# Kernel optimization log

Hardware: AMD Instinct MI355X
Metric: run time of the kernel (lower is better)

## Reference

```python
import jax, jax.numpy as jnp
import numpy as np

N_NODES = 50000
N_EDGES = 800000
D = 128
BN_EPS = 1e-5


def swish(h):
    return h * jax.nn.sigmoid(h)


def linear_bn_swish(h, W, b, g, be):
    # Linear -> BatchNorm1d (training stats, biased var) -> Swish
    h = h @ W + b
    mean = jnp.mean(h, axis=0)
    var = jnp.mean((h - mean) ** 2, axis=0)
    h = (h - mean) * jax.lax.rsqrt(var + BN_EPS) * g + be
    return swish(h)


def setup_inputs() -> dict:
    key = jax.random.key(0)
    ks = jax.random.split(key, 8)
    scale = 1.0 / np.sqrt(D)
    return {
        "x": jax.random.normal(ks[0], (N_NODES, D), dtype=jnp.float32),
        "vals": jax.random.uniform(ks[1], (N_EDGES,), dtype=jnp.float32),
        "W1": jax.random.normal(ks[2], (D, D), dtype=jnp.float32) * scale,
        "b1": jnp.zeros((D,), dtype=jnp.float32),
        "g1": jnp.ones((D,), dtype=jnp.float32),
        "be1": jnp.zeros((D,), dtype=jnp.float32),
        "W2": jax.random.normal(ks[3], (D, D), dtype=jnp.float32) * scale,
        "b2": jnp.zeros((D,), dtype=jnp.float32),
        "g2": jnp.ones((D,), dtype=jnp.float32),
        "be2": jnp.zeros((D,), dtype=jnp.float32),
        "eps": jnp.zeros((1,), dtype=jnp.float32),
        "rows": jax.random.randint(ks[4], (N_EDGES,), 0, N_NODES, dtype=jnp.int32),
        "cols": jax.random.randint(ks[5], (N_EDGES,), 0, N_NODES, dtype=jnp.int32),
    }


def reference(x, vals, W1, b1, g1, be1, W2, b2, g2, be2, eps, rows, cols):
    # out = spmm(adj, x): gather neighbor features, scale by edge weight, scatter-add to rows
    msgs = vals[:, None] * x[cols]                                   # [E, D]
    agg = jax.ops.segment_sum(msgs, rows, num_segments=x.shape[0])   # [N, D]
    h = agg + (1.0 + eps[0]) * x
    h = linear_bn_swish(h, W1, b1, g1, be1)
    h = linear_bn_swish(h, W2, b2, g2, be2)
    return h
```

## Files before the change

### kernel.cpp

```cpp
#include <hip/hip_runtime.h>

#define D 128
#define DH 64
#define BR 64
#define BSH 6
#define NBMAX 1024
#define FCAP 2048
#define GT 512
#define CH 4096
#define SCT 512
#define TS 68

typedef float f32x4 __attribute__((ext_vector_type(4)));
typedef short s16x8 __attribute__((ext_vector_type(8)));

static __device__ __forceinline__ unsigned short f2bf(float f) {
    unsigned u = __float_as_uint(f);
    u += 0x7FFF + ((u >> 16) & 1);
    return (unsigned short)(u >> 16);
}
static __device__ __forceinline__ float bflo(unsigned u) { return __uint_as_float(u << 16); }
static __device__ __forceinline__ float bfhi(unsigned u) { return __uint_as_float(u & 0xFFFF0000u); }
static __device__ __forceinline__ float bf2f(short v) {
    return __uint_as_float(((unsigned)(unsigned short)v) << 16);
}

__global__ __launch_bounds__(256)
void k_setup(const float* __restrict__ x, unsigned* __restrict__ xh, int total4,
             const float* __restrict__ W1, const float* __restrict__ W2,
             unsigned short* __restrict__ Wsw1, unsigned short* __restrict__ Wsw2,
             int* __restrict__ ccur, float* __restrict__ stats, int eb) {
    int bid = blockIdx.x, t = threadIdx.x;
    if (bid < eb) {
        int i = bid * 256 + t;
        if (i < total4) {
            float4 v = ((const float4*)x)[i];
            uint2 o;
            o.x = (unsigned)f2bf(v.x) | ((unsigned)f2bf(v.y) << 16);
            o.y = (unsigned)f2bf(v.z) | ((unsigned)f2bf(v.w) << 16);
            ((uint2*)xh)[i] = o;
        }
    } else if (bid < eb + 16) {
        int gidx = (bid - eb) * 256 + t;
        const float* W = (gidx < 2048) ? W1 : W2;
        unsigned short* Wsw = (gidx < 2048) ? Wsw1 : Wsw2;
        int idx = gidx & 2047;
        int lane = idx & 63, nt = (idx >> 6) & 7, kt = idx >> 9;
        int k0 = kt * 32 + (lane >> 4) * 8;
        int n = nt * 16 + (lane & 15);
        unsigned short* dst = &Wsw[(size_t)((kt * 8 + nt) * 64 + lane) * 8];
#pragma unroll
        for (int j = 0; j < 8; ++j) dst[j] = f2bf(W[(k0 + j) * D + n]);
    } else {
        if (t < 512) stats[t] = 0.f;
        for (int i = t; i < NBMAX; i += 256) ccur[i] = 0;
    }
}

__global__ __launch_bounds__(SCT)
void k_cscatter(const int* __restrict__ rows, const int* __restrict__ cols,
                const float* __restrict__ vals, int* __restrict__ gcur,
                uint2* __restrict__ sedge, int E) {
    __shared__ int lcnt[NBMAX];
    __shared__ int lbase[NBMAX];
    __shared__ int gbase[NBMAX];
    __shared__ uint2 sl[CH];
    __shared__ unsigned short sbkt[CH];
    int t = threadIdx.x;
    int base = blockIdx.x * CH;
    int tot = min(E - base, CH);

    for (int i = t; i < NBMAX; i += SCT) lcnt[i] = 0;
    __syncthreads();

    int r[8]; unsigned c[8], v[8];
#pragma unroll
    for (int j = 0; j < 8; ++j) {
        int e = base + j * SCT + t;
        if (e < E) {
            r[j] = rows[e];
            c[j] = (unsigned)cols[e];
            v[j] = __float_as_uint(vals[e]);
            atomicAdd(&lcnt[r[j] >> BSH], 1);
        } else r[j] = -1;
    }
    __syncthreads();

    lbase[t] = lcnt[t];
    lbase[t + SCT] = lcnt[t + SCT];
    __syncthreads();
    for (int d = 1; d < NBMAX; d <<= 1) {
        int a0 = (t >= d) ? lbase[t - d] : 0;
        int i1 = t + SCT;
        int a1 = (i1 >= d) ? lbase[i1 - d] : 0;
        __syncthreads();
        lbase[t] += a0;
        lbase[i1] += a1;
        __syncthreads();
    }
#pragma unroll
    for (int k = 0; k < 2; ++k) {
        int i = t + k * SCT;
        int cnt = lcnt[i];
        gbase[i] = cnt ? atomicAdd(&gcur[i], cnt) : 0;
        lbase[i] -= cnt;
    }
    __syncthreads();
    for (int i = t; i < NBMAX; i += SCT) lcnt[i] = 0;
    __syncthreads();

#pragma unroll
    for (int j = 0; j < 8; ++j) {
        if (r[j] >= 0) {
            int b = r[j] >> BSH;
            int p = lbase[b] + atomicAdd(&lcnt[b], 1);
            sl[p] = make_uint2(c[j] | ((unsigned)(r[j] & (BR - 1)) << 16), v[j]);
            sbkt[p] = (unsigned short)b;
        }
    }
    __syncthreads();

#pragma unroll
    for (int j = 0; j < 8; ++j) {
        int i = j * SCT + t;
        if (i < tot) {
            int b = sbkt[i];
            int pos = gbase[b] + (i - lbase[b]);
            if (pos < FCAP) sedge[(size_t)b * FCAP + pos] = sl[i];
        }
    }
}

__global__ __launch_bounds__(GT, 8)
void k_sgg(const uint2* __restrict__ sedge, const int* __restrict__ ccur,
           const unsigned* __restrict__ xh, const float* __restrict__ eps,
           const unsigned short* __restrict__ Wsw, const float* __restrict__ bias,
           unsigned short* __restrict__ Hout, float* __restrict__ stats, int N) {
    __shared__ int cnt[BR], sbase[BR], cur[BR];
    __shared__ __align__(16) unsigned char uAbuf[64 * TS * 4];
    __shared__ uint2 ebufB[FCAP];
    __shared__ float redS[8 * 64];
    __shared__ float redQ[8 * 64];
    uint2* ebufA = (uint2*)uAbuf;
    unsigned* tile = (unsigned*)uAbuf;

    int b = blockIdx.x, t = threadIdx.x;
    size_t e0 = (size_t)b * FCAP;
    int cntE = ccur[b];
    if (cntE > FCAP) cntE = FCAP;
    if (t < BR) { cnt[t] = 0; cur[t] = 0; }
    __syncthreads();
    for (int i = t; i < cntE; i += GT) {
        uint2 ed = sedge[e0 + i];
        ebufA[i] = ed;
        atomicAdd(&cnt[ed.x >> 16], 1);
    }
    __syncthreads();
    if (t < BR) sbase[t] = cnt[t];
    __syncthreads();
    for (int d = 1; d < BR; d <<= 1) {
        int add = (t < BR && t >= d) ? sbase[t - d] : 0;
        __syncthreads();
        if (t < BR) sbase[t] += add;
        __syncthreads();
    }
    if (t < BR) sbase[t] -= cnt[t];
    __syncthreads();
    for (int i = t; i < cntE; i += GT) {
        uint2 ed = ebufA[i];
        int r = ed.x >> 16;
        int p = sbase[r] + atomicAdd(&cur[r], 1);
        ebufB[p] = make_uint2(ed.x & 0xFFFFu, ed.y);
    }
    __syncthreads();

    int lane = t & 63, w = t >> 6;
    float s = 1.0f + eps[0];
    int row0 = b * BR;
    for (int rl = w; rl < BR; rl += 8) {
        int grow = row0 + rl;
        if (grow >= N) { tile[rl * TS + lane] = 0; continue; }
        unsigned u = xh[(size_t)grow * DH + lane];
        float ax = s * bflo(u), ay = s * bfhi(u);
        int i = sbase[rl];
        int i1 = (rl < BR - 1) ? sbase[rl + 1] : cntE;
        for (; i + 8 <= i1; i += 8) {
            uint2 ed[8];
            unsigned uu[8];
#pragma unroll
            for (int j = 0; j < 8; ++j) ed[j] = ebufB[i + j];
#pragma unroll
            for (int j = 0; j < 8; ++j) uu[j] = xh[(size_t)ed[j].x * DH + lane];
#pragma unroll
            for (int j = 0; j < 8; ++j) {
                float v = __uint_as_float(ed[j].y);
                ax += v * bflo(uu[j]);
                ay += v * bfhi(uu[j]);
            }
        }
        for (; i < i1; ++i) {
            uint2 ed = ebufB[i];
            unsigned uu = xh[(size_t)ed.x * DH + lane];
            float v = __uint_as_float(ed.y);
            ax += v * bflo(uu);
            ay += v * bfhi(uu);
        }
        tile[rl * TS + lane] = (unsigned)f2bf(ax) | ((unsigned)f2bf(ay) << 16);
    }
    __syncthreads();

    int m = lane & 15, quad = lane >> 4;
    int wr = w & 3, wc = w >> 2;
    int arowl = wr * 16 + m;

    f32x4 acc[4];
#pragma unroll
    for (int ntl = 0; ntl < 4; ++ntl) acc[ntl] = (f32x4){0.f, 0.f, 0.f, 0.f};

    const s16x8* wp = (const s16x8*)Wsw;
#pragma unroll
    for (int kt = 0; kt < 4; ++kt) {
        s16x8 a = *(const s16x8*)&tile[arowl * TS + kt * 16 + quad * 4];
#pragma unroll
        for (int ntl = 0; ntl < 4; ++ntl) {
            int nt = wc * 4 + ntl;
            s16x8 bf = wp[(kt * 8 + nt) * 64 + lane];
            acc[ntl] = __builtin_amdgcn_mfma_f32_16x16x32_bf16(a, bf, acc[ntl], 0, 0, 0);
        }
    }

#pragma unroll
    for (int ntl = 0; ntl < 4; ++ntl) {
        int nt = wc * 4 + ntl;
        float bv = bias[nt * 16 + m];
        float ss = 0.f, q = 0.f;
#pragma unroll
        for (int r = 0; r < 4; ++r) {
            int row = row0 + wr * 16 + quad * 4 + r;
            float h = acc[ntl][r] + bv;
            if (row < N) {
                Hout[(size_t)row * D + nt * 16 + m] = f2bf(h);
                ss += h; q += h * h;
            }
        }
        ss += __shfl_xor(ss, 16, 64); ss += __shfl_xor(ss, 32, 64);
        q += __shfl_xor(q, 16, 64);   q += __shfl_xor(q, 32, 64);
        if (quad == 0) {
            redS[w * 64 + ntl * 16 + m] = ss;
            redQ[w * 64 + ntl * 16 + m] = q;
        }
    }
    __syncthreads();
    if (t < D) {
        int ch = t >> 6, cl = t & 63;
        float ts = 0.f, tq = 0.f;
#pragma unroll
        for (int wr2 = 0; wr2 < 4; ++wr2) {
            ts += redS[(ch * 4 + wr2) * 64 + cl];
            tq += redQ[(ch * 4 + wr2) * 64 + cl];
        }
        atomicAdd(&stats[t], ts);
        atomicAdd(&stats[D + t], tq);
    }
}

__global__ __launch_bounds__(256)
void k_gemm2f(const unsigned short* __restrict__ H1, const unsigned short* __restrict__ Wsw,
              const float* __restrict__ bias, const float* __restrict__ stats1,
              const float* __restrict__ g1, const float* __restrict__ be1, float invN,
              unsigned short* __restrict__ Hout, float* __restrict__ stats2, int N) {
    __shared__ float redS[4 * D];
    __shared__ float redQ[4 * D];
    __shared__ float sa[D], sb[D];
    int tid = threadIdx.x, lane = tid & 63, w = tid >> 6;
    if (tid < D) {
        float mean = stats1[tid] * invN;
        float var = fmaxf(stats1[D + tid] * invN - mean * mean, 0.f);
        float a = g1[tid] * rsqrtf(var + 1e-5f);
        sa[tid] = a;
        sb[tid] = be1[tid] - mean * a;
    }
    __syncthreads();

    int row0 = blockIdx.x * 64 + w * 16;
    int m = lane & 15, quad = lane >> 4;

    f32x4 acc[8];
#pragma unroll
    for (int nt = 0; nt < 8; ++nt) acc[nt] = (f32x4){0.f, 0.f, 0.f, 0.f};

    int arow = row0 + m;
    bool avalid = arow < N;
    const s16x8* wp = (const s16x8*)Wsw;
    s16x8 az = {0, 0, 0, 0, 0, 0, 0, 0};
#pragma unroll
    for (int kt = 0; kt < 4; ++kt) {
        s16x8 a = az;
        if (avalid) {
            s16x8 raw = *(const s16x8*)&H1[(size_t)arow * D + kt * 32 + quad * 8];
#pragma unroll
            for (int j = 0; j < 8; ++j) {
                int k = kt * 32 + quad * 8 + j;
                float dd = bf2f(raw[j]) * sa[k] + sb[k];
                float o = dd / (1.f + __expf(-dd));
                a[j] = (short)f2bf(o);
            }
        }
#pragma unroll
        for (int nt = 0; nt < 8; ++nt) {
            s16x8 b = wp[(kt * 8 + nt) * 64 + lane];
            acc[nt] = __builtin_amdgcn_mfma_f32_16x16x32_bf16(a, b, acc[nt], 0, 0, 0);
        }
    }

#pragma unroll
    for (int nt = 0; nt < 8; ++nt) {
        float bv = bias[nt * 16 + m];
        float s = 0.f, q = 0.f;
#pragma unroll
        for (int r = 0; r < 4; ++r) {
            int row = row0 + quad * 4 + r;
            float h = acc[nt][r] + bv;
            if (row < N) {
                Hout[(size_t)row * D + nt * 16 + m] = f2bf(h);
                s += h; q += h * h;
            }
        }
        s += __shfl_xor(s, 16, 64); s += __shfl_xor(s, 32, 64);
        q += __shfl_xor(q, 16, 64); q += __shfl_xor(q, 32, 64);
        if (quad == 0) {
            redS[w * D + nt * 16 + m] = s;
            redQ[w * D + nt * 16 + m] = q;
        }
    }
    __syncthreads();
    if (tid < D) {
        float ts = redS[tid] + redS[D + tid] + redS[2 * D + tid] + redS[3 * D + tid];
        float tq = redQ[tid] + redQ[D + tid] + redQ[2 * D + tid] + redQ[3 * D + tid];
        atomicAdd(&stats2[tid], ts);
        atomicAdd(&stats2[D + tid], tq);
    }
}

__global__ void k_bnswish(const unsigned* __restrict__ inh, float* __restrict__ outp,
                          const float* __restrict__ stats, const float* __restrict__ g,
                          const float* __restrict__ be, float invN, int total4) {
    __shared__ float sa[D], sb[D];
    int j = threadIdx.x;
    if (j < D) {
        float mean = stats[j] * invN;
        float var = fmaxf(stats[D + j] * invN - mean * mean, 0.f);
        float a = g[j] * rsqrtf(var + 1e-5f);
        sa[j] = a;
        sb[j] = be[j] - mean * a;
    }
    __syncthreads();
    int i = blockIdx.x * blockDim.x + threadIdx.x;
    if (i >= total4) return;
    uint2 u = ((const uint2*)inh)[i];
    int c = (i * 4) & (D - 1);
    float d0 = bflo(u.x) * sa[c + 0] + sb[c + 0];
    float d1 = bfhi(u.x) * sa[c + 1] + sb[c + 1];
    float d2 = bflo(u.y) * sa[c + 2] + sb[c + 2];
    float d3 = bfhi(u.y) * sa[c + 3] + sb[c + 3];
    float o0 = d0 / (1.f + __expf(-d0));
    float o1 = d1 / (1.f + __expf(-d1));
    float o2 = d2 / (1.f + __expf(-d2));
    float o3 = d3 / (1.f + __expf(-d3));
    ((float4*)outp)[i] = make_float4(o0, o1, o2, o3);
}

extern "C" void kernel_launch(void* const* d_in, const int* in_sizes, int n_in,
                              void* d_out, int out_size, void* d_ws, size_t ws_size,
                              hipStream_t stream) {
    const float* x    = (const float*)d_in[0];
    const float* vals = (const float*)d_in[1];
    const float* W1   = (const float*)d_in[2];
    const float* b1   = (const float*)d_in[3];
    const float* g1   = (const float*)d_in[4];
    const float* be1  = (const float*)d_in[5];
    const float* W2   = (const float*)d_in[6];
    const float* b2   = (const float*)d_in[7];
    const float* g2   = (const float*)d_in[8];
    const float* be2  = (const float*)d_in[9];
    const float* eps  = (const float*)d_in[10];
    const int*  rows  = (const int*)d_in[11];
    const int*  cols  = (const int*)d_in[12];
    float* out = (float*)d_out;

    int N = in_sizes[0] / D;
    int E = in_sizes[1];
    int nb = (N + BR - 1) / BR;

    char* p = (char*)d_ws;
    float* stats = (float*)p;              p += 4 * D * sizeof(float);
    int* ccur = (int*)p;                   p += (size_t)NBMAX * sizeof(int);
    p = (char*)(((uintptr_t)p + 15) & ~(uintptr_t)15);
    unsigned short* Wsw1 = (unsigned short*)p; p += (size_t)D * D * 2;
    unsigned short* Wsw2 = (unsigned short*)p; p += (size_t)D * D * 2;
    p = (char*)(((uintptr_t)p + 15) & ~(uintptr_t)15);
    uint2* sedge  = (uint2*)p;             p += (size_t)nb * FCAP * sizeof(uint2);
    unsigned* xh = (unsigned*)p;           p += (size_t)N * DH * sizeof(unsigned);
    unsigned* h1 = (unsigned*)p;

    float* stats1 = stats;
    float* stats2 = stats + 2 * D;

    int total4 = N * D / 4;
    int eb = (total4 + 255) / 256;
    int gblk = (N + 63) / 64;
    float invN = 1.0f / (float)N;
    int scb = (E + CH - 1) / CH;

    k_setup<<<eb + 17, 256, 0, stream>>>(x, xh, total4, W1, W2, Wsw1, Wsw2,
                                         ccur, stats, eb);
    k_cscatter<<<scb, SCT, 0, stream>>>(rows, cols, vals, ccur, sedge, E);
    k_sgg<<<nb, GT, 0, stream>>>(sedge, ccur, xh, eps, Wsw1, b1,
                                 (unsigned short*)h1, stats1, N);
    k_gemm2f<<<gblk, 256, 0, stream>>>((const unsigned short*)h1, Wsw2, b2,
                                       stats1, g1, be1, invN,
                                       (unsigned short*)xh, stats2, N);
    k_bnswish<<<eb, 256, 0, stream>>>(xh, out, stats2, g2, be2, invN, total4);
}
```

Before: 210.2 us.

## Rebalance scatter chunks, use warp-shuffle scan, and widen gather unroll to 16

The bucket-scatter kernel now splits the edges evenly over about 256 blocks instead of fixed 4096-edge chunks. Its 1024-entry prefix scan is replaced by a per-thread serial sum plus a single-wavefront shuffle scan, which removes many barrier rounds. In the fused gather+GEMM kernel, the 8-wide unrolled edge loop with a scalar tail becomes a predicated 16-wide loop, putting more gathers in flight, and the launch-bound occupancy hint drops from 8 to 6 to allow more registers. Trade-offs: padded lanes do wasted gathers, there is less occupancy to hide latency, and each scatter block handles slightly fewer edges.

```diff
diff --git a/kernel.cpp b/kernel.cpp
--- a/kernel.cpp
+++ b/kernel.cpp
@@ -60,15 +60,16 @@
 __global__ __launch_bounds__(SCT)
 void k_cscatter(const int* __restrict__ rows, const int* __restrict__ cols,
                 const float* __restrict__ vals, int* __restrict__ gcur,
-                uint2* __restrict__ sedge, int E) {
+                uint2* __restrict__ sedge, int E, int chunk) {
     __shared__ int lcnt[NBMAX];
     __shared__ int lbase[NBMAX];
     __shared__ int gbase[NBMAX];
     __shared__ uint2 sl[CH];
     __shared__ unsigned short sbkt[CH];
     int t = threadIdx.x;
-    int base = blockIdx.x * CH;
-    int tot = min(E - base, CH);
+    int base = blockIdx.x * chunk;
+    int tot = min(E - base, chunk);
+    if (tot <= 0) return;
 
     for (int i = t; i < NBMAX; i += SCT) lcnt[i] = 0;
     __syncthreads();
@@ -76,8 +77,9 @@
     int r[8]; unsigned c[8], v[8];
 #pragma unroll
     for (int j = 0; j < 8; ++j) {
-        int e = base + j * SCT + t;
-        if (e < E) {
+        int o = j * SCT + t;
+        if (o < tot) {
+            int e = base + o;
             r[j] = rows[e];
             c[j] = (unsigned)cols[e];
             v[j] = __float_as_uint(vals[e]);
@@ -86,27 +88,30 @@
     }
     __syncthreads();
 
-    lbase[t] = lcnt[t];
-    lbase[t + SCT] = lcnt[t + SCT];
-    __syncthreads();
-    for (int d = 1; d < NBMAX; d <<= 1) {
-        int a0 = (t >= d) ? lbase[t - d] : 0;
-        int i1 = t + SCT;
-        int a1 = (i1 >= d) ? lbase[i1 - d] : 0;
-        __syncthreads();
-        lbase[t] += a0;
-        lbase[i1] += a1;
-        __syncthreads();
-    }
-#pragma unroll
-    for (int k = 0; k < 2; ++k) {
-        int i = t + k * SCT;
+    if (t < 64) {
+        int part[16], s = 0;
+#pragma unroll
+        for (int k = 0; k < 16; ++k) {
+            part[k] = s;
+            s += lcnt[t * 16 + k];
+        }
+        int incl = s;
+#pragma unroll
+        for (int d = 1; d < 64; d <<= 1) {
+            int n = __shfl_up(incl, d, 64);
+            if (t >= d) incl += n;
+        }
+        int excl = incl - s;
+#pragma unroll
+        for (int k = 0; k < 16; ++k) lbase[t * 16 + k] = excl + part[k];
+    }
+    __syncthreads();
+
+    for (int i = t; i < NBMAX; i += SCT) {
         int cnt = lcnt[i];
         gbase[i] = cnt ? atomicAdd(&gcur[i], cnt) : 0;
-        lbase[i] -= cnt;
-    }
-    __syncthreads();
-    for (int i = t; i < NBMAX; i += SCT) lcnt[i] = 0;
+        lcnt[i] = 0;
+    }
     __syncthreads();
 
 #pragma unroll
@@ -131,7 +136,7 @@
     }
 }
 
-__global__ __launch_bounds__(GT, 8)
+__global__ __launch_bounds__(GT, 6)
 void k_sgg(const uint2* __restrict__ sedge, const int* __restrict__ ccur,
            const unsigned* __restrict__ xh, const float* __restrict__ eps,
            const unsigned short* __restrict__ Wsw, const float* __restrict__ bias,
@@ -182,28 +187,22 @@
         if (grow >= N) { tile[rl * TS + lane] = 0; continue; }
         unsigned u = xh[(size_t)grow * DH + lane];
         float ax = s * bflo(u), ay = s * bfhi(u);
-        int i = sbase[rl];
+        int i0 = sbase[rl];
         int i1 = (rl < BR - 1) ? sbase[rl + 1] : cntE;
-        for (; i + 8 <= i1; i += 8) {
-            uint2 ed[8];
-            unsigned uu[8];
-#pragma unroll
-            for (int j = 0; j < 8; ++j) ed[j] = ebufB[i + j];
-#pragma unroll
-            for (int j = 0; j < 8; ++j) uu[j] = xh[(size_t)ed[j].x * DH + lane];
-#pragma unroll
-            for (int j = 0; j < 8; ++j) {
-                float v = __uint_as_float(ed[j].y);
-                ax += v * bflo(uu[j]);
-                ay += v * bfhi(uu[j]);
+        for (int i = i0; i < i1; i += 16) {
+            unsigned uu[16]; float vv[16];
+#pragma unroll
+            for (int j = 0; j < 16; ++j) {
+                int idx = (i + j < i1) ? (i + j) : (i1 - 1);
+                uint2 ed = ebufB[idx];
+                vv[j] = (i + j < i1) ? __uint_as_float(ed.y) : 0.f;
+                uu[j] = xh[(size_t)ed.x * DH + lane];
             }
-        }
-        for (; i < i1; ++i) {
-            uint2 ed = ebufB[i];
-            unsigned uu = xh[(size_t)ed.x * DH + lane];
-            float v = __uint_as_float(ed.y);
-            ax += v * bflo(uu);
-            ay += v * bfhi(uu);
+#pragma unroll
+            for (int j = 0; j < 16; ++j) {
+                ax += vv[j] * bflo(uu[j]);
+                ay += vv[j] * bfhi(uu[j]);
+            }
         }
         tile[rl * TS + lane] = (unsigned)f2bf(ax) | ((unsigned)f2bf(ay) << 16);
     }
@@ -410,11 +409,13 @@
     int eb = (total4 + 255) / 256;
     int gblk = (N + 63) / 64;
     float invN = 1.0f / (float)N;
-    int scb = (E + CH - 1) / CH;
+    int scb = 256;
+    int chunk = (E + scb - 1) / scb;
+    if (chunk > CH) { scb = (E + CH - 1) / CH; chunk = (E + scb - 1) / scb; }
 
     k_setup<<<eb + 17, 256, 0, stream>>>(x, xh, total4, W1, W2, Wsw1, Wsw2,
                                          ccur, stats, eb);
-    k_cscatter<<<scb, SCT, 0, stream>>>(rows, cols, vals, ccur, sedge, E);
+    k_cscatter<<<scb, SCT, 0, stream>>>(rows, cols, vals, ccur, sedge, E, chunk);
     k_sgg<<<nb, GT, 0, stream>>>(sedge, ccur, xh, eps, Wsw1, b1,
                                  (unsigned short*)h1, stats1, N);
     k_gemm2f<<<gblk, 256, 0, stream>>>((const unsigned short*)h1, Wsw2, b2,
```

Measured after the change: 223.7 us. 6.4% more time.

## Halve row-bucket size to 32 and replace bucket prefix scan with wave scan

Applied to the files above, without the earlier changes.

Row buckets shrink from 64 to 32 rows, which doubles the number of buckets and halves the per-bucket edge capacity. The fused gather+GEMM kernel therefore runs twice as many blocks with smaller shared-memory footprints, and its MFMA warp tiling is remapped to 2x4 with the stats reduction adjusted to match. The scatter kernel's 1024-entry block-wide Hillis-Steele scan is replaced by a single-wavefront scan: each thread does a serial 32-element partial sum, then a shuffle scan. This removes many __syncthreads rounds. The trade-offs are more blocks, more global-counter atomics and more overflow risk, since about 512 expected edges per bucket now sit against a cap of 1024.

```diff
diff --git a/kernel.cpp b/kernel.cpp
--- a/kernel.cpp
+++ b/kernel.cpp
@@ -2,10 +2,10 @@
 
 #define D 128
 #define DH 64
-#define BR 64
-#define BSH 6
-#define NBMAX 1024
-#define FCAP 2048
+#define BR 32
+#define BSH 5
+#define NBMAX 2048
+#define FCAP 1024
 #define GT 512
 #define CH 4096
 #define SCT 512
@@ -86,27 +86,30 @@
     }
     __syncthreads();
 
-    lbase[t] = lcnt[t];
-    lbase[t + SCT] = lcnt[t + SCT];
-    __syncthreads();
-    for (int d = 1; d < NBMAX; d <<= 1) {
-        int a0 = (t >= d) ? lbase[t - d] : 0;
-        int i1 = t + SCT;
-        int a1 = (i1 >= d) ? lbase[i1 - d] : 0;
-        __syncthreads();
-        lbase[t] += a0;
-        lbase[i1] += a1;
-        __syncthreads();
-    }
-#pragma unroll
-    for (int k = 0; k < 2; ++k) {
-        int i = t + k * SCT;
+    if (t < 64) {
+        int part[32], s = 0;
+#pragma unroll
+        for (int k = 0; k < 32; ++k) {
+            part[k] = s;
+            s += lcnt[t * 32 + k];
+        }
+        int incl = s;
+#pragma unroll
+        for (int d = 1; d < 64; d <<= 1) {
+            int n = __shfl_up(incl, d, 64);
+            if (t >= d) incl += n;
+        }
+        int excl = incl - s;
+#pragma unroll
+        for (int k = 0; k < 32; ++k) lbase[t * 32 + k] = excl + part[k];
+    }
+    __syncthreads();
+
+    for (int i = t; i < NBMAX; i += SCT) {
         int cnt = lcnt[i];
         gbase[i] = cnt ? atomicAdd(&gcur[i], cnt) : 0;
-        lbase[i] -= cnt;
-    }
-    __syncthreads();
-    for (int i = t; i < NBMAX; i += SCT) lcnt[i] = 0;
+        lcnt[i] = 0;
+    }
     __syncthreads();
 
 #pragma unroll
@@ -137,10 +140,10 @@
            const unsigned short* __restrict__ Wsw, const float* __restrict__ bias,
            unsigned short* __restrict__ Hout, float* __restrict__ stats, int N) {
     __shared__ int cnt[BR], sbase[BR], cur[BR];
-    __shared__ __align__(16) unsigned char uAbuf[64 * TS * 4];
+    __shared__ __align__(16) unsigned char uAbuf[BR * TS * 4];
     __shared__ uint2 ebufB[FCAP];
-    __shared__ float redS[8 * 64];
-    __shared__ float redQ[8 * 64];
+    __shared__ float redS[8 * 32];
+    __shared__ float redQ[8 * 32];
     uint2* ebufA = (uint2*)uAbuf;
     unsigned* tile = (unsigned*)uAbuf;
 
@@ -210,28 +213,28 @@
     __syncthreads();
 
     int m = lane & 15, quad = lane >> 4;
-    int wr = w & 3, wc = w >> 2;
+    int wr = w & 1, wc = w >> 1;
     int arowl = wr * 16 + m;
 
-    f32x4 acc[4];
-#pragma unroll
-    for (int ntl = 0; ntl < 4; ++ntl) acc[ntl] = (f32x4){0.f, 0.f, 0.f, 0.f};
+    f32x4 acc[2];
+#pragma unroll
+    for (int ntl = 0; ntl < 2; ++ntl) acc[ntl] = (f32x4){0.f, 0.f, 0.f, 0.f};
 
     const s16x8* wp = (const s16x8*)Wsw;
 #pragma unroll
     for (int kt = 0; kt < 4; ++kt) {
         s16x8 a = *(const s16x8*)&tile[arowl * TS + kt * 16 + quad * 4];
 #pragma unroll
-        for (int ntl = 0; ntl < 4; ++ntl) {
-            int nt = wc * 4 + ntl;
+        for (int ntl = 0; ntl < 2; ++ntl) {
+            int nt = wc * 2 + ntl;
             s16x8 bf = wp[(kt * 8 + nt) * 64 + lane];
             acc[ntl] = __builtin_amdgcn_mfma_f32_16x16x32_bf16(a, bf, acc[ntl], 0, 0, 0);
         }
     }
 
 #pragma unroll
-    for (int ntl = 0; ntl < 4; ++ntl) {
-        int nt = wc * 4 + ntl;
+    for (int ntl = 0; ntl < 2; ++ntl) {
+        int nt = wc * 2 + ntl;
         float bv = bias[nt * 16 + m];
         float ss = 0.f, q = 0.f;
 #pragma unroll
@@ -246,18 +249,20 @@
         ss += __shfl_xor(ss, 16, 64); ss += __shfl_xor(ss, 32, 64);
         q += __shfl_xor(q, 16, 64);   q += __shfl_xor(q, 32, 64);
         if (quad == 0) {
-            redS[w * 64 + ntl * 16 + m] = ss;
-            redQ[w * 64 + ntl * 16 + m] = q;
+            redS[w * 32 + ntl * 16 + m] = ss;
+            redQ[w * 32 + ntl * 16 + m] = q;
         }
     }
     __syncthreads();
     if (t < D) {
-        int ch = t >> 6, cl = t & 63;
+        int nt = t >> 4, m2 = t & 15;
+        int wc2 = nt >> 1, ntl2 = nt & 1;
         float ts = 0.f, tq = 0.f;
 #pragma unroll
-        for (int wr2 = 0; wr2 < 4; ++wr2) {
-            ts += redS[(ch * 4 + wr2) * 64 + cl];
-            tq += redQ[(ch * 4 + wr2) * 64 + cl];
+        for (int wr2 = 0; wr2 < 2; ++wr2) {
+            int ww = wc2 * 2 + wr2;
+            ts += redS[ww * 32 + ntl2 * 16 + m2];
+            tq += redQ[ww * 32 + ntl2 * 16 + m2];
         }
         atomicAdd(&stats[t], ts);
         atomicAdd(&stats[D + t], tq);
```

Result: slower. 221.1 us (+5.2%).
